# Kernel tuning notes

Hardware: AMD Instinct MI355X
Metric: run time of the kernel (lower is better)

## Reference

```python
import jax, jax.numpy as jnp
import numpy as np

TEMP = 0.5
A_LC = 1.0


def setup_inputs() -> dict:
    key = jax.random.key(0)
    kx, kl = jax.random.split(key)
    b, nviews, d = 8192, 2, 128
    x = jax.random.normal(kx, (b, nviews, d), dtype=jnp.float32)
    labels = jax.random.randint(kl, (b,), 0, 10, dtype=jnp.int64)
    return {"x": x, "labels": labels}


def reference(x, labels):
    # x: [b, 2, d]; labels: [b]
    # Defaults: log_first=True, old_lnew=False, detect_noise=False,
    # pos_in_denom=False, K=-1, noise_rate=0, a_spread=0, lc_norm=False.
    # Only view pair (ii=1, jj=0) contributes; pairs = 1.
    vi = x[:, 1, :]  # [b, d]
    vj = x[:, 0, :]  # [b, d]
    num = jnp.einsum('bd,cd->bc', vi, vj) / TEMP  # [b, b]

    pos = labels[:, None] == labels[None, :]  # [b, b] same-class (incl. self)
    neg = ~pos

    # logsumexp over each row's negatives (stable, masked)
    neg_num = jnp.where(neg, num, -jnp.inf)
    L_neg = jax.nn.logsumexp(neg_num, axis=1)  # [b]

    # denominator[i] = sum_{p in pos(i)} logsumexp([num[i,p], num[i, negs(i)]])
    #               = sum_{p in pos(i)} logaddexp(num[i,p], L_neg[i])
    lae = jnp.logaddexp(num, L_neg[:, None])  # [b, b]
    denominator = jnp.where(pos, lae, 0.0).sum(axis=1)  # [b]
    numerator = -jnp.where(pos, num, 0.0).sum(axis=1)   # [b]

    div_factor = pos.sum(axis=1).astype(num.dtype)  # |pos(i)| >= 1
    log_prob = numerator + denominator
    a = A_LC * log_prob / div_factor
    pairs = 1.0
    return a.mean() / pairs
```

## Files before the change

### kernel.cpp

```cpp
#include <hip/hip_runtime.h>
#include <hip/hip_bf16.h>
#include <math.h>

#define DDIM 128
#define JS 32
#define ROWS_BLK 128
#define NCLS 10
#define TMAX 16
#define CMAX 128.0f
#define LOG2E 1.44269504f
#define LN2F 0.69314718f
#define MBIAS (-CMAX * LOG2E)

typedef __attribute__((ext_vector_type(8))) short short8;
typedef __attribute__((ext_vector_type(4))) float f32x4;

__device__ __forceinline__ ushort f2bf(float f) {
    union { float f; unsigned u; } v; v.f = f;
    unsigned r = (v.u + 0x7FFFu + ((v.u >> 16) & 1u)) >> 16;
    return (ushort)r;
}

__device__ __forceinline__ void gload_lds16(const ushort* g, ushort* l) {
    __builtin_amdgcn_global_load_lds(
        (const __attribute__((address_space(1))) unsigned int*)g,
        (__attribute__((address_space(3))) unsigned int*)l,
        16, 0, 0);
}

__global__ __launch_bounds__(256) void convert_kernel(
    const float* __restrict__ x, ushort* __restrict__ vi, ushort* __restrict__ vj, int B)
{
    int t = blockIdx.x * 256 + threadIdx.x;
    int r = t >> 5;
    int k4 = (t & 31) * 4;
    if (r >= B) return;
    float4 a = *reinterpret_cast<const float4*>(x + (size_t)r * 256 + DDIM + k4);
    float4 b = *reinterpret_cast<const float4*>(x + (size_t)r * 256 + k4);
    ushort4 ua, ub;
    ua.x = f2bf(a.x * 2.0f); ua.y = f2bf(a.y * 2.0f); ua.z = f2bf(a.z * 2.0f); ua.w = f2bf(a.w * 2.0f);
    ub.x = f2bf(b.x); ub.y = f2bf(b.y); ub.z = f2bf(b.z); ub.w = f2bf(b.w);
    *reinterpret_cast<ushort4*>(vi + (size_t)r * DDIM + k4) = ua;
    *reinterpret_cast<ushort4*>(vj + (size_t)r * DDIM + k4) = ub;
}

__global__ __launch_bounds__(1024) void build_index_kernel(
    const int* __restrict__ labels, int* __restrict__ idx, int* __restrict__ counts, int B)
{
    const int c = blockIdx.x;
    const int tid = threadIdx.x;
    const int wave = tid >> 6, lane = tid & 63;
    __shared__ int base;
    __shared__ int wsum[16];
    if (tid == 0) base = 0;
    __syncthreads();
    for (int start = 0; start < B; start += 1024) {
        bool m = (labels[start + tid] == c);
        unsigned long long mask = __ballot(m);
        int lrank = __popcll(mask & ((1ull << lane) - 1ull));
        if (lane == 0) wsum[wave] = __popcll(mask);
        __syncthreads();
        int wbase = 0, total = 0;
        #pragma unroll
        for (int w = 0; w < 16; ++w) {
            if (w < wave) wbase += wsum[w];
            total += wsum[w];
        }
        int b0 = base;
        __syncthreads();
        if (m) idx[c * B + b0 + wbase + lrank] = start + tid;
        if (tid == 0) base = b0 + total;
        __syncthreads();
    }
    if (tid == 0) counts[c] = base;
}

__global__ __launch_bounds__(256, 4) void pass1_kernel(
    const ushort* __restrict__ vi, const ushort* __restrict__ vj,
    const int* __restrict__ labels, float* __restrict__ os, int B)
{
    __shared__ ushort lbuf[2][16 * DDIM];

    const int tid = threadIdx.x;
    const int wave = tid >> 6, lane = tid & 63;
    const int col16 = lane & 15, grp = lane >> 4;
    const int nbr = B / ROWS_BLK;
    const int rb = blockIdx.x % nbr;
    const int chunk = blockIdx.x / nbr;
    const int ri0 = rb * ROWS_BLK + wave * 32;
    const int jchunk = B / JS;
    const int j0 = chunk * jchunk;
    const int NG = jchunk / 16;

    short8 afrag[8];
    #pragma unroll
    for (int h = 0; h < 2; ++h)
        #pragma unroll
        for (int ks = 0; ks < 4; ++ks)
            afrag[h * 4 + ks] = *reinterpret_cast<const short8*>(
                vi + (size_t)(ri0 + h * 16 + col16) * DDIM + ks * 32 + grp * 8);

    int rl[8];
    float s[8];
    #pragma unroll
    for (int r = 0; r < 8; ++r) {
        int row = ri0 + (r >> 2) * 16 + grp * 4 + (r & 3);
        rl[r] = labels[row];
        s[r] = 0.0f;
    }

    const int lrow  = wave * 4 + (lane >> 4);
    const int lslot = lane & 15;
    const int gslot = lslot ^ (lrow & 7);

    auto STAGE = [&](int g, int b) {
        int jb = j0 + g * 16;
        gload_lds16(vj + (size_t)(jb + lrow) * DDIM + gslot * 8,
                    &lbuf[b][(wave * 4) * DDIM]);
    };
    auto COMP = [&](int b, int cl) {
        short8 bfrag[4];
        #pragma unroll
        for (int ks = 0; ks < 4; ++ks) {
            int p = (ks * 4 + grp) ^ (col16 & 7);
            bfrag[ks] = *reinterpret_cast<const short8*>(&lbuf[b][col16 * DDIM + p * 8]);
        }
        #pragma unroll
        for (int h = 0; h < 2; ++h) {
            f32x4 acc = (f32x4){0.f, 0.f, 0.f, 0.f};
            #pragma unroll
            for (int ks = 0; ks < 4; ++ks)
                acc = __builtin_amdgcn_mfma_f32_16x16x32_bf16(afrag[h * 4 + ks], bfrag[ks], acc, 0, 0, 0);
            #pragma unroll
            for (int rr = 0; rr < 4; ++rr) {
                int r = h * 4 + rr;
                float e = exp2f(fmaf(acc[rr], LOG2E, MBIAS));
                e = (cl == rl[r]) ? 0.0f : e;
                s[r] += e;
            }
        }
    };

    STAGE(0, 0);
    int clcur = labels[j0 + col16];
    __syncthreads();
    for (int g = 0; g < NG; ++g) {
        int b = g & 1;
        int clnext = clcur;
        if (g + 1 < NG) {
            STAGE(g + 1, b ^ 1);
            clnext = labels[j0 + (g + 1) * 16 + col16];
        }
        COMP(b, clcur);
        clcur = clnext;
        __syncthreads();
    }

    #pragma unroll
    for (int r = 0; r < 8; ++r) {
        for (int off = 8; off; off >>= 1) s[r] += __shfl_xor(s[r], off);
        if (col16 == 0) {
            int row = ri0 + (r >> 2) * 16 + grp * 4 + (r & 3);
            os[chunk * B + row] = s[r];
        }
    }
}

__global__ __launch_bounds__(256) void merge_sneg_kernel(
    const float* __restrict__ os, float* __restrict__ sneg, int B)
{
    int i = blockIdx.x * 256 + threadIdx.x;
    if (i >= B) return;
    float s = 0.0f;
    #pragma unroll
    for (int h = 0; h < JS; ++h) s += os[h * B + i];
    sneg[i] = s;
}

__global__ __launch_bounds__(256) void pass2_kernel(
    const ushort* __restrict__ vi, const ushort* __restrict__ vj,
    const int* __restrict__ idx, const int* __restrict__ counts,
    const float* __restrict__ sneg,
    float* __restrict__ p, int B)
{
    const int c  = blockIdx.x / TMAX;
    const int rt = blockIdx.x % TMAX;
    const int qt = blockIdx.y;
    const int n  = counts[c];
    if (rt * 64 >= n || qt * 64 >= n) return;
    const int tid = threadIdx.x;
    const int wave = tid >> 6, lane = tid & 63;
    const int col16 = lane & 15, grp = lane >> 4;
    const int* cidx = idx + c * B;

    for (int rt2 = rt; rt2 * 64 < n; rt2 += TMAX) {
        const int ri0 = rt2 * 64 + wave * 16;
        int aslot = ri0 + col16;
        int aid = cidx[aslot < n ? aslot : n - 1];
        short8 afrag[4];
        #pragma unroll
        for (int ks = 0; ks < 4; ++ks)
            afrag[ks] = *reinterpret_cast<const short8*>(
                vi + (size_t)aid * DDIM + ks * 32 + grp * 8);

        bool rv[4];
        int rid[4];
        float sn[4], s[4];
        #pragma unroll
        for (int r = 0; r < 4; ++r) {
            int slot = ri0 + grp * 4 + r;
            rv[r] = slot < n;
            rid[r] = cidx[slot < n ? slot : n - 1];
            sn[r] = sneg[rid[r]];
            s[r] = 0.0f;
        }

        for (int qt2 = qt; qt2 * 64 < n; qt2 += TMAX) {
            const int jb = qt2 * 64;
            bool jv[4];
            int cid[4];
            f32x4 acc[4];
            #pragma unroll
            for (int cg = 0; cg < 4; ++cg) {
                int slot = jb + cg * 16 + col16;
                jv[cg] = slot < n;
                cid[cg] = cidx[slot < n ? slot : n - 1];
                acc[cg] = (f32x4){0.f, 0.f, 0.f, 0.f};
            }
            #pragma unroll
            for (int cg = 0; cg < 4; ++cg) {
                #pragma unroll
                for (int ks = 0; ks < 4; ++ks) {
                    short8 bfrag = *reinterpret_cast<const short8*>(
                        vj + (size_t)cid[cg] * DDIM + ks * 32 + grp * 8);
                    acc[cg] = __builtin_amdgcn_mfma_f32_16x16x32_bf16(afrag[ks], bfrag, acc[cg], 0, 0, 0);
                }
            }
            #pragma unroll
            for (int r = 0; r < 4; ++r) {
                #pragma unroll
                for (int cg = 0; cg < 4; ++cg) {
                    float v = acc[cg][r];
                    float e = exp2f(fmaf(v, LOG2E, MBIAS));
                    float d = fmaf(__log2f(e + sn[r] + 1e-38f), LN2F, CMAX) - v;
                    if (jv[cg]) s[r] += d;
                }
            }
        }

        #pragma unroll
        for (int r = 0; r < 4; ++r) {
            for (int off = 8; off; off >>= 1) s[r] += __shfl_xor(s[r], off);
            if (col16 == 0 && rv[r]) p[qt * B + rid[r]] = s[r];
        }
    }
}

__global__ __launch_bounds__(256) void merge_pass2_kernel(
    const int* __restrict__ labels, const int* __restrict__ counts,
    const float* __restrict__ p, double* __restrict__ part, int B)
{
    int i = blockIdx.x * 256 + threadIdx.x;
    int n = counts[labels[i]];
    int ntq = (n + 63) >> 6;
    if (ntq > TMAX) ntq = TMAX;
    float s = 0.0f;
    for (int q = 0; q < ntq; ++q) s += p[q * B + i];
    double contrib = (double)(s / (float)n);
    __shared__ double red[256];
    red[threadIdx.x] = contrib;
    __syncthreads();
    for (int off = 128; off; off >>= 1) {
        if (threadIdx.x < off) red[threadIdx.x] += red[threadIdx.x + off];
        __syncthreads();
    }
    if (threadIdx.x == 0) part[blockIdx.x] = red[0];
}

__global__ __launch_bounds__(64) void finalize_kernel(
    const double* __restrict__ part, float* __restrict__ out, int nparts, int B)
{
    __shared__ double red[64];
    double v = (threadIdx.x < nparts) ? part[threadIdx.x] : 0.0;
    red[threadIdx.x] = v;
    __syncthreads();
    for (int off = 32; off; off >>= 1) {
        if (threadIdx.x < off) red[threadIdx.x] += red[threadIdx.x + off];
        __syncthreads();
    }
    if (threadIdx.x == 0) out[0] = (float)(red[0] / (double)B);
}

extern "C" void kernel_launch(void* const* d_in, const int* in_sizes, int n_in,
                              void* d_out, int out_size, void* d_ws, size_t ws_size,
                              hipStream_t stream) {
    const float* x      = (const float*)d_in[0];
    const int*   labels = (const int*)d_in[1];
    int B = in_sizes[1];
    float* out = (float*)d_out;

    ushort* vi     = (ushort*)d_ws;
    ushort* vj     = vi + (size_t)B * DDIM;
    float*  os     = (float*)(vj + (size_t)B * DDIM);
    float*  p      = os;
    float*  sneg   = os + (size_t)JS * B;
    int*    idx    = (int*)(sneg + B);
    int*    counts = idx + (size_t)NCLS * B;
    double* part   = (double*)(counts + 64);

    convert_kernel<<<dim3(B * 32 / 256), dim3(256), 0, stream>>>(x, vi, vj, B);
    build_index_kernel<<<dim3(NCLS), dim3(1024), 0, stream>>>(labels, idx, counts, B);

    int nbr = B / ROWS_BLK;
    pass1_kernel<<<dim3(nbr * JS), dim3(256), 0, stream>>>(vi, vj, labels, os, B);
    merge_sneg_kernel<<<dim3((B + 255) / 256), dim3(256), 0, stream>>>(os, sneg, B);
    pass2_kernel<<<dim3(NCLS * TMAX, TMAX), dim3(256), 0, stream>>>(vi, vj, idx, counts, sneg, p, B);
    merge_pass2_kernel<<<dim3(B / 256), dim3(256), 0, stream>>>(labels, counts, p, part, B);
    finalize_kernel<<<dim3(1), dim3(64), 0, stream>>>(part, out, B / 256, B);
}
```

Baseline: 88.06 us.

## Deepen pass1 LDS pipeline to four buffers with explicit vmcnt waits

Replaces the double-buffered LDS staging in pass1 with a four-slot ring that prefetches two groups ahead. Each iteration issues a manual s_waitcnt vmcnt plus a single s_barrier instead of a full __syncthreads after compute. All column labels are preloaded into registers up front rather than loaded one per iteration. The aim is to hide global-to-LDS latency and cut barrier cost. In exchange it uses more LDS and registers, and its correctness depends on the vmcnt counts matching the outstanding loads (the label loads also count against vmcnt), and on NG not exceeding NGMAX.

Result: faster. 85.46 us (-3.0%).

```diff
diff --git a/kernel.cpp b/kernel.cpp
--- a/kernel.cpp
+++ b/kernel.cpp
@@ -5,6 +5,7 @@
 #define DDIM 128
 #define JS 32
 #define ROWS_BLK 128
+#define NGMAX 16
 #define NCLS 10
 #define TMAX 16
 #define CMAX 128.0f
@@ -79,7 +80,7 @@
     const ushort* __restrict__ vi, const ushort* __restrict__ vj,
     const int* __restrict__ labels, float* __restrict__ os, int B)
 {
-    __shared__ ushort lbuf[2][16 * DDIM];
+    __shared__ ushort lbuf[4][16 * DDIM];
 
     const int tid = threadIdx.x;
     const int wave = tid >> 6, lane = tid & 63;
@@ -109,21 +110,28 @@
         s[r] = 0.0f;
     }
 
+    int cl[NGMAX];
+    #pragma unroll
+    for (int g = 0; g < NGMAX; ++g)
+        cl[g] = labels[j0 + g * 16 + col16];
+
     const int lrow  = wave * 4 + (lane >> 4);
     const int lslot = lane & 15;
     const int gslot = lslot ^ (lrow & 7);
 
-    auto STAGE = [&](int g, int b) {
+    auto STAGE = [&](int g) {
         int jb = j0 + g * 16;
         gload_lds16(vj + (size_t)(jb + lrow) * DDIM + gslot * 8,
-                    &lbuf[b][(wave * 4) * DDIM]);
+                    &lbuf[g & 3][(wave * 4) * DDIM]);
     };
-    auto COMP = [&](int b, int cl) {
+    auto COMP = [&](int g) {
+        const ushort* buf = lbuf[g & 3];
+        int clg = cl[g];
         short8 bfrag[4];
         #pragma unroll
         for (int ks = 0; ks < 4; ++ks) {
             int p = (ks * 4 + grp) ^ (col16 & 7);
-            bfrag[ks] = *reinterpret_cast<const short8*>(&lbuf[b][col16 * DDIM + p * 8]);
+            bfrag[ks] = *reinterpret_cast<const short8*>(&buf[col16 * DDIM + p * 8]);
         }
         #pragma unroll
         for (int h = 0; h < 2; ++h) {
@@ -135,25 +143,25 @@
             for (int rr = 0; rr < 4; ++rr) {
                 int r = h * 4 + rr;
                 float e = exp2f(fmaf(acc[rr], LOG2E, MBIAS));
-                e = (cl == rl[r]) ? 0.0f : e;
+                e = (clg == rl[r]) ? 0.0f : e;
                 s[r] += e;
             }
         }
     };
 
-    STAGE(0, 0);
-    int clcur = labels[j0 + col16];
-    __syncthreads();
+    STAGE(0);
+    STAGE(1);
     for (int g = 0; g < NG; ++g) {
-        int b = g & 1;
-        int clnext = clcur;
-        if (g + 1 < NG) {
-            STAGE(g + 1, b ^ 1);
-            clnext = labels[j0 + (g + 1) * 16 + col16];
-        }
-        COMP(b, clcur);
-        clcur = clnext;
-        __syncthreads();
+        if (g + 2 < NG) {
+            STAGE(g + 2);
+            asm volatile("s_waitcnt vmcnt(2)" ::: "memory");
+        } else if (g + 1 < NG) {
+            asm volatile("s_waitcnt vmcnt(1)" ::: "memory");
+        } else {
+            asm volatile("s_waitcnt vmcnt(0)" ::: "memory");
+        }
+        asm volatile("s_barrier" ::: "memory");
+        COMP(g);
     }
 
     #pragma unroll
```
